# Optimization experiments

Measured on AMD Instinct MI355X. Metric: run time of the kernel, lower is better.

The kernel has to match this reference:

```python
import jax, jax.numpy as jnp
import numpy as np

REGION_DIM = 144
LLM_DIM = 3584
NUM_HEADS = 4
HEAD_DIM = REGION_DIM // NUM_HEADS          # 36
V_HEAD_DIM = LLM_DIM // NUM_HEADS           # 896
LN_EPS = 1e-5
N, M = 4096, 4096


def setup_inputs() -> dict:
    key = jax.random.key(0)
    ks = jax.random.split(key, 16)
    s = 0.02
    return {
        "target_emb": jax.random.normal(ks[0], (N, REGION_DIM), jnp.float32),
        "source_emb": jax.random.normal(ks[1], (M, LLM_DIM), jnp.float32),
        "value_emb":  jax.random.normal(ks[2], (M, LLM_DIM), jnp.float32),
        # params stored [in, out] (transposed vs torch nn.Linear)
        "wq_w": jax.random.normal(ks[3], (REGION_DIM, REGION_DIM), jnp.float32) * s,
        "wq_b": jnp.zeros((REGION_DIM,), jnp.float32),
        "wk_w": jax.random.normal(ks[4], (LLM_DIM, REGION_DIM), jnp.float32) * s,
        "wk_b": jnp.zeros((REGION_DIM,), jnp.float32),
        # per-head V projections stacked: [H, llm_dim, llm_dim//H]
        "wv_w": jax.random.normal(ks[5], (NUM_HEADS, LLM_DIM, V_HEAD_DIM), jnp.float32) * s,
        "wv_b": jnp.zeros((NUM_HEADS, V_HEAD_DIM), jnp.float32),
        "resid_w": jax.random.normal(ks[6], (REGION_DIM, LLM_DIM), jnp.float32) * s,
        "resid_b": jnp.zeros((LLM_DIM,), jnp.float32),
        "out_w": jax.random.normal(ks[7], (LLM_DIM, LLM_DIM), jnp.float32) * s,
        "out_b": jnp.zeros((LLM_DIM,), jnp.float32),
        "ln_g": jnp.ones((LLM_DIM,), jnp.float32),
        "ln_b": jnp.zeros((LLM_DIM,), jnp.float32),
    }


def reference(target_emb, source_emb, value_emb,
              wq_w, wq_b, wk_w, wk_b, wv_w, wv_b,
              resid_w, resid_b, out_w, out_b, ln_g, ln_b):
    n = target_emb.shape[0]
    # Q: [N, region_dim] -> [H, N, head_dim]; K: [M, llm_dim] -> [H, M, head_dim]
    Q = (target_emb @ wq_w + wq_b).reshape(n, NUM_HEADS, HEAD_DIM).transpose(1, 0, 2)
    K = (source_emb @ wk_w + wk_b).reshape(-1, NUM_HEADS, HEAD_DIM).transpose(1, 0, 2)
    scores = jnp.einsum('hnd,hmd->hnm', Q, K) / jnp.sqrt(jnp.float32(HEAD_DIM))
    attn = jax.nn.softmax(scores, axis=-1)      # dropout = identity (eval mode)
    # per-head value projections: [H, M, llm_dim//H]
    V = jnp.einsum('me,hed->hmd', value_emb, wv_w) + wv_b[:, None, :]
    ctx = jnp.einsum('hnm,hmd->nhd', attn, V).reshape(n, LLM_DIM)
    x = ctx + (target_emb @ resid_w + resid_b)   # residual_proj (region_dim != llm_dim)
    mu = jnp.mean(x, axis=-1, keepdims=True)
    var = jnp.mean(jnp.square(x - mu), axis=-1, keepdims=True)
    x = (x - mu) * jax.lax.rsqrt(var + LN_EPS) * ln_g + ln_b
    return x @ out_w + out_b
```

## Files before the change

### kernel.cpp

```cpp
#include <hip/hip_runtime.h>

typedef _Float16 f16;
typedef _Float16 f16x8 __attribute__((ext_vector_type(8)));
typedef float f32x4 __attribute__((ext_vector_type(4)));

#define REGION_DIM 144
#define LLM_DIM 3584
#define NUM_HEADS 4
#define HEAD_DIM 36
#define HEAD_PAD 64
#define QK_COLS 256
#define KPAD_REGION 160
#define V_HEAD 896
#define LN_EPS 1e-5f

__device__ __forceinline__ void gl_lds16(const f16* g, f16* l)
{
    __builtin_amdgcn_global_load_lds(
        (const __attribute__((address_space(1))) unsigned int*)g,
        (__attribute__((address_space(3))) unsigned int*)l, 16, 0, 0);
}

#define S_BARRIER() do { asm volatile("" ::: "memory"); __builtin_amdgcn_s_barrier(); asm volatile("" ::: "memory"); } while (0)
#define SCHED_FENCE() __builtin_amdgcn_sched_barrier(0)

__global__ void k_convert_pad(const float* __restrict__ in, f16* __restrict__ out,
                              int Cin, int Cout)
{
    int r = blockIdx.y;
    int c = blockIdx.x * 256 + threadIdx.x;
    if (c >= Cout) return;
    float v = (c < Cin) ? in[(long)r * Cin + c] : 0.f;
    out[(long)r * Cout + c] = (f16)v;
}

__global__ void k_transpose(const float* __restrict__ in, f16* __restrict__ out,
                            int R, int C, int Rpad, int Cpad,
                            long in_bstride, long out_bstride)
{
    __shared__ float tile[32][33];
    const float* ip = in + (long)blockIdx.z * in_bstride;
    f16* op = out + (long)blockIdx.z * out_bstride;
    int r0 = blockIdx.y * 32, c0 = blockIdx.x * 32;
    int tx = threadIdx.x, ty = threadIdx.y;
#pragma unroll
    for (int i = 0; i < 32; i += 8) {
        int r = r0 + ty + i, c = c0 + tx;
        tile[ty + i][tx] = (r < R && c < C) ? ip[(long)r * C + c] : 0.f;
    }
    __syncthreads();
#pragma unroll
    for (int i = 0; i < 32; i += 8) {
        int c = c0 + ty + i, r = r0 + tx;
        if (c < Cpad && r < Rpad) op[(long)c * Rpad + r] = (f16)tile[tx][ty + i];
    }
}

__global__ void k_headpad_w(const float* __restrict__ w, const float* __restrict__ b,
                            f16* __restrict__ outW, float* __restrict__ outB,
                            int E, int Epad)
{
    int hp = blockIdx.y;
    int h = hp >> 6, kk = hp & 63;
    int d = h * HEAD_DIM + kk;
    bool valid = (kk < HEAD_DIM);
    int e = blockIdx.x * 256 + threadIdx.x;
    if (e < Epad) {
        float v = (valid && e < E) ? w[(long)e * REGION_DIM + d] : 0.f;
        outW[(long)hp * Epad + e] = (f16)v;
    }
    if (blockIdx.x == 0 && threadIdx.x == 0) outB[hp] = valid ? b[d] : 0.f;
}

enum { EPI_F16_EXPSCALE = 0,
       EPI_F16_BIASROW  = 1,
       EPI_F16_DIVROW   = 2,
       EPI_F32_BIASCOL  = 3,
       EPI_F16_BIASCOL  = 4,
       EPI_F16_EXPSUM   = 5 };

template <int EPI>
__global__ __launch_bounds__(256, 2)
void gemm_f16(const f16* __restrict__ A, int lda, long sAz,
              const f16* __restrict__ Bt, int ldb, long sBz,
              void* __restrict__ Cv, int ldc, long sCz,
              const float* __restrict__ bias, long sbz, float scale, int K,
              float* __restrict__ rowpart)
{
    __shared__ __align__(16) f16 sA[128 * 32];
    __shared__ __align__(16) f16 sB[128 * 32];
    __shared__ float ps[256];
    const int tid = threadIdx.x;
    const int z = blockIdx.z;
    A += (long)z * sAz;
    Bt += (long)z * sBz;
    if (bias) bias += (long)z * sbz;

    const int gx = gridDim.x, gy = gridDim.y;
    int pid = blockIdx.y * gx + blockIdx.x;
    const int GROUP = 8;
    int span = GROUP * gx;
    int gid = pid / span;
    int y0 = gid * GROUP;
    int gsz = (gy - y0 < GROUP) ? (gy - y0) : GROUP;
    int rem = pid - gid * span;
    const int by = y0 + rem % gsz;
    const int bx = rem / gsz;
    const int m0 = by * 128, n0 = bx * 128;

    const int w = tid >> 6, l = tid & 63;
    const int wu = __builtin_amdgcn_readfirstlane(w);
    const int wr = w >> 1, wc = w & 1;

    f32x4 acc[4][4] = {};

    const int srow = tid >> 2;
    const int scol = (tid & 3) * 8;
    const f16* Ag = A + (long)(m0 + srow) * lda + scol;
    const f16* Bg = Bt + (long)(n0 + srow) * ldb + scol;
    f16* sA0 = sA + wu * 512;
    f16* sA1 = sA + 2048 + wu * 512;
    f16* sB0 = sB + wu * 512;
    f16* sB1 = sB + 2048 + wu * 512;
    const int qk = (l >> 4) * 8;
    const int fr = l & 15;

    for (int k0 = 0; k0 < K; k0 += 32) {
        __syncthreads();
        gl_lds16(Ag + k0, sA0);
        gl_lds16(Ag + (long)64 * lda + k0, sA1);
        gl_lds16(Bg + k0, sB0);
        gl_lds16(Bg + (long)64 * ldb + k0, sB1);
        __syncthreads();

        f16x8 af[4], bf[4];
#pragma unroll
        for (int mt = 0; mt < 4; mt++)
            af[mt] = *(const f16x8*)&sA[(wr * 64 + mt * 16 + fr) * 32 + qk];
#pragma unroll
        for (int nt = 0; nt < 4; nt++)
            bf[nt] = *(const f16x8*)&sB[(wc * 64 + nt * 16 + fr) * 32 + qk];
#pragma unroll
        for (int mt = 0; mt < 4; mt++)
#pragma unroll
            for (int nt = 0; nt < 4; nt++)
                acc[mt][nt] = __builtin_amdgcn_mfma_f32_16x16x32_f16(af[mt], bf[nt], acc[mt][nt], 0, 0, 0);
    }

    const int q4 = (l >> 4) * 4;
    float bc[4];
#pragma unroll
    for (int nt = 0; nt < 4; nt++) {
        if constexpr (EPI == EPI_F16_BIASCOL || EPI == EPI_F32_BIASCOL)
            bc[nt] = bias[n0 + wc * 64 + nt * 16 + fr];
        else
            bc[nt] = 0.f;
    }
    float rsum[4][4];
    if constexpr (EPI == EPI_F16_EXPSUM) {
#pragma unroll
        for (int a = 0; a < 4; a++)
#pragma unroll
            for (int b = 0; b < 4; b++) rsum[a][b] = 0.f;
    }
#pragma unroll
    for (int mt = 0; mt < 4; mt++)
#pragma unroll
        for (int r = 0; r < 4; r++) {
            int row = m0 + wr * 64 + mt * 16 + q4 + r;
            float rowv = 0.f;
            if constexpr (EPI == EPI_F16_BIASROW) rowv = bias[row];
            if constexpr (EPI == EPI_F16_DIVROW) rowv = 1.f / bias[row];
#pragma unroll
            for (int nt = 0; nt < 4; nt++) {
                int col = n0 + wc * 64 + nt * 16 + fr;
                float v = acc[mt][nt][r];
                if constexpr (EPI == EPI_F16_EXPSCALE || EPI == EPI_F16_EXPSUM) {
                    float e = __expf(v * scale);
                    ((f16*)Cv + (long)z * sCz)[(long)row * ldc + col] = (f16)e;
                    if constexpr (EPI == EPI_F16_EXPSUM) rsum[mt][r] += e;
                } else if constexpr (EPI == EPI_F16_BIASROW) {
                    ((f16*)Cv + (long)z * sCz)[(long)row * ldc + col] = (f16)(v + rowv);
                } else if constexpr (EPI == EPI_F16_DIVROW) {
                    ((f16*)Cv + (long)z * sCz)[(long)row * ldc + col] = (f16)(v * rowv);
                } else if constexpr (EPI == EPI_F16_BIASCOL) {
                    ((f16*)Cv + (long)z * sCz)[(long)row * ldc + col] = (f16)(v + bc[nt]);
                } else {
                    ((float*)Cv + (long)z * sCz)[(long)row * ldc + col] = v + bc[nt];
                }
            }
        }

    if constexpr (EPI == EPI_F16_EXPSUM) {
#pragma unroll
        for (int mt = 0; mt < 4; mt++)
#pragma unroll
            for (int r = 0; r < 4; r++) {
                float s = rsum[mt][r];
                s += __shfl_xor(s, 1);
                s += __shfl_xor(s, 2);
                s += __shfl_xor(s, 4);
                s += __shfl_xor(s, 8);
                if (fr == 0) ps[wc * 128 + wr * 64 + mt * 16 + q4 + r] = s;
            }
        __syncthreads();
        if (tid < 128) {
            long rows = (long)gy * 128;
            rowpart[((long)z * gx + bx) * rows + m0 + tid] = ps[tid] + ps[128 + tid];
        }
    }
}

template <int EPI>
__global__ __launch_bounds__(512, 2)
void gemm256_f16(const f16* __restrict__ A, int lda,
                 const f16* __restrict__ Bt, int ldb,
                 void* __restrict__ Cv, int ldc,
                 const float* __restrict__ bias, int K)
{
    __shared__ __align__(16) f16 sm[65536];
    f16* smf = sm;

    const int tid = threadIdx.x;
    const int l = tid & 63;

    const int gx = gridDim.x, gy = gridDim.y;
    int pid = blockIdx.y * gx + blockIdx.x;
    int nwg = gx * gy;
    int q = nwg >> 3, r8 = nwg & 7;
    int xcd = pid & 7, idx = pid >> 3;
    int swz = (xcd < r8) ? (xcd * (q + 1) + idx)
                         : (r8 * (q + 1) + (xcd - r8) * q + idx);
    const int by = swz % gy, bx = swz / gy;
    const int m0 = by * 256, n0 = bx * 256;

    const int wu = __builtin_amdgcn_readfirstlane(tid >> 6);
    const int wr = wu >> 2;
    const int wc = wu & 3;
    const int wst = wu * 512;

    const int strow = wu * 8 + (l >> 3);
    const int stcol = ((l & 7) ^ (l >> 3)) * 8;
    const f16* Asrc = A + (size_t)(m0 + strow) * lda + stcol;
    const f16* Bsrc = Bt + (size_t)(n0 + strow) * ldb + stcol;

    const int fr = l & 15;
    const int hi8 = (l >> 4) * 8;
    const int swl = (fr & 7) * 8;
    const int ca0 = hi8 ^ swl;
    const int ca1 = (32 + hi8) ^ swl;

    const int NT = K >> 6;

    f32x4 acc[8][4] = {};
    f16x8 af0[4][2], af1[4][2], bf0[2][2], bf1[2][2];

    gl_lds16(Asrc, smf + wst);
    gl_lds16(Asrc + (size_t)64 * lda, smf + 4096 + wst);
    gl_lds16(Asrc + (size_t)128 * lda, smf + 8192 + wst);
    gl_lds16(Asrc + (size_t)192 * lda, smf + 8192 + 4096 + wst);
    gl_lds16(Bsrc, smf + 16384 + wst);
    gl_lds16(Bsrc + (size_t)64 * ldb, smf + 16384 + 4096 + wst);
    gl_lds16(Bsrc + (size_t)128 * ldb, smf + 16384 + 8192 + wst);
    gl_lds16(Bsrc + (size_t)192 * ldb, smf + 16384 + 8192 + 4096 + wst);
    if (NT > 1) {
        gl_lds16(Bsrc + 64, smf + 32768 + 16384 + wst);
        gl_lds16(Bsrc + 64 + (size_t)64 * ldb, smf + 32768 + 16384 + 4096 + wst);
        gl_lds16(Asrc + 64, smf + 32768 + wst);
        gl_lds16(Asrc + 64 + (size_t)64 * lda, smf + 32768 + 4096 + wst);
        asm volatile("s_waitcnt vmcnt(4)" ::: "memory");
    } else {
        asm volatile("s_waitcnt vmcnt(0)" ::: "memory");
    }
    S_BARRIER();
    {
        const f16* sAp0 = smf + wr * 8192 + fr * 64;
#pragma unroll
        for (int i = 0; i < 4; i++) {
            af0[i][0] = *(const f16x8*)(sAp0 + i * 1024 + ca0);
            af0[i][1] = *(const f16x8*)(sAp0 + i * 1024 + ca1);
        }
    }

#define MFMA_Q(MB, NB, AF, BF)                                                        \
    _Pragma("unroll") for (int i = 0; i < 4; i++)                                     \
    _Pragma("unroll") for (int j = 0; j < 2; j++) {                                   \
        acc[MB + i][NB + j] = __builtin_amdgcn_mfma_f32_16x16x32_f16(                 \
            AF[i][0], BF[j][0], acc[MB + i][NB + j], 0, 0, 0);                        \
        acc[MB + i][NB + j] = __builtin_amdgcn_mfma_f32_16x16x32_f16(                 \
            AF[i][1], BF[j][1], acc[MB + i][NB + j], 0, 0, 0);                        \
    }

    for (int t = 0; t < NT; ++t) {
        const int p = t & 1;
        const f16* sAp = smf + (p << 15) + wr * 8192 + fr * 64;
        const f16* sBp = smf + (p << 15) + 16384 + wc * 4096 + fr * 64;
        const bool s1 = (t + 1 < NT), s2 = (t + 2 < NT);

#pragma unroll
        for (int j = 0; j < 2; j++) {
            bf0[j][0] = *(const f16x8*)(sBp + j * 1024 + ca0);
            bf0[j][1] = *(const f16x8*)(sBp + j * 1024 + ca1);
        }
#pragma unroll
        for (int j = 0; j < 2; j++) {
            bf1[j][0] = *(const f16x8*)(sBp + 2048 + j * 1024 + ca0);
            bf1[j][1] = *(const f16x8*)(sBp + 2048 + j * 1024 + ca1);
        }
        if (s1) {
            const f16* sa = Asrc + (size_t)128 * lda + (size_t)(t + 1) * 64;
            f16* da = smf + ((p ^ 1) << 15) + 8192 + wst;
            gl_lds16(sa, da);
            gl_lds16(sa + (size_t)64 * lda, da + 4096);
            const f16* sb = Bsrc + (size_t)128 * ldb + (size_t)(t + 1) * 64;
            f16* db = smf + ((p ^ 1) << 15) + 16384 + 8192 + wst;
            gl_lds16(sb, db);
            gl_lds16(sb + (size_t)64 * ldb, db + 4096);
        }
        asm volatile("s_waitcnt lgkmcnt(4)" ::: "memory");
        SCHED_FENCE();
        __builtin_amdgcn_s_setprio(1);
        MFMA_Q(0, 0, af0, bf0);
        __builtin_amdgcn_s_setprio(0);

#pragma unroll
        for (int i = 0; i < 4; i++) {
            af1[i][0] = *(const f16x8*)(sAp + 4096 + i * 1024 + ca0);
            af1[i][1] = *(const f16x8*)(sAp + 4096 + i * 1024 + ca1);
        }
        asm volatile("s_waitcnt lgkmcnt(8)" ::: "memory");
        SCHED_FENCE();
        __builtin_amdgcn_s_setprio(1);
        MFMA_Q(0, 2, af0, bf1);
        __builtin_amdgcn_s_setprio(0);

        S_BARRIER();
        if (s2) {
            const f16* sb = Bsrc + (size_t)(t + 2) * 64;
            f16* db = smf + (p << 15) + 16384 + wst;
            gl_lds16(sb, db);
            gl_lds16(sb + (size_t)64 * ldb, db + 4096);
        }
        asm volatile("s_waitcnt lgkmcnt(0)" ::: "memory");
        SCHED_FENCE();
        __builtin_amdgcn_s_setprio(1);
        MFMA_Q(4, 2, af1, bf1);
        __builtin_amdgcn_s_setprio(0);

        S_BARRIER();
        if (s2) {
            const f16* sa = Asrc + (size_t)(t + 2) * 64;
            f16* da = smf + (p << 15) + wst;
            gl_lds16(sa, da);
            gl_lds16(sa + (size_t)64 * lda, da + 4096);
            asm volatile("s_waitcnt vmcnt(4)" ::: "memory");
        } else if (s1) {
            asm volatile("s_waitcnt vmcnt(0)" ::: "memory");
        }
        if (s1) {
            S_BARRIER();
            const f16* sApN = smf + ((p ^ 1) << 15) + wr * 8192 + fr * 64;
#pragma unroll
            for (int i = 0; i < 4; i++) {
                af0[i][0] = *(const f16x8*)(sApN + i * 1024 + ca0);
                af0[i][1] = *(const f16x8*)(sApN + i * 1024 + ca1);
            }
        }
        __builtin_amdgcn_s_setprio(1);
        MFMA_Q(4, 0, af1, bf0);
        __builtin_amdgcn_s_setprio(0);
    }
#undef MFMA_Q

    const int q4 = (l >> 4) * 4;
    float bc[4];
#pragma unroll
    for (int nt = 0; nt < 4; nt++) {
        if constexpr (EPI == EPI_F16_BIASCOL || EPI == EPI_F32_BIASCOL)
            bc[nt] = bias[n0 + wc * 64 + nt * 16 + fr];
        else
            bc[nt] = 0.f;
    }
#pragma unroll
    for (int mt = 0; mt < 8; mt++)
#pragma unroll
        for (int r = 0; r < 4; r++) {
            int row = m0 + wr * 128 + mt * 16 + q4 + r;
            float rowv = 0.f;
            if constexpr (EPI == EPI_F16_BIASROW) rowv = bias[row];
            if constexpr (EPI == EPI_F16_DIVROW) rowv = 1.f / bias[row];
#pragma unroll
            for (int nt = 0; nt < 4; nt++) {
                int col = n0 + wc * 64 + nt * 16 + fr;
                float v = acc[mt][nt][r];
                if constexpr (EPI == EPI_F16_BIASROW) {
                    ((f16*)Cv)[(size_t)row * ldc + col] = (f16)(v + rowv);
                } else if constexpr (EPI == EPI_F16_DIVROW) {
                    ((f16*)Cv)[(size_t)row * ldc + col] = (f16)(v * rowv);
                } else if constexpr (EPI == EPI_F16_BIASCOL) {
                    ((f16*)Cv)[(size_t)row * ldc + col] = (f16)(v + bc[nt]);
                } else {
                    ((float*)Cv)[(size_t)row * ldc + col] = v + bc[nt];
                }
            }
        }
}

__global__ __launch_bounds__(512, 2)
void gemm_pv(const f16* __restrict__ A, int lda, long sAz,
             const f16* __restrict__ Bt, int ldb, long sBz,
             f16* __restrict__ C, int ldc, long sCz,
             const float* __restrict__ lsum, long slz, int K)
{
    __shared__ __align__(16) f16 sm[49152];
    const int tid = threadIdx.x;
    const int l = tid & 63;
    const int z = blockIdx.z;
    A += (size_t)z * sAz;
    Bt += (size_t)z * sBz;
    C += (size_t)z * sCz;
    lsum += (size_t)z * slz;

    const int gx = gridDim.x, gy = gridDim.y;
    int pid = blockIdx.y * gx + blockIdx.x;
    int nwg = gx * gy;
    int q = nwg >> 3, r8 = nwg & 7;
    int xcd = pid & 7, idx = pid >> 3;
    int swz = (xcd < r8) ? (xcd * (q + 1) + idx)
                         : (r8 * (q + 1) + (xcd - r8) * q + idx);
    const int by = swz % gy, bx = swz / gy;
    const int m0 = by * 256, n0 = bx * 128;

    const int wu = __builtin_amdgcn_readfirstlane(tid >> 6);
    const int wr = wu >> 1;
    const int wc = wu & 1;
    const int wst = wu * 512;

    const int strow = wu * 8 + (l >> 3);
    const int stcol = ((l & 7) ^ (l >> 3)) * 8;
    const f16* Asrc = A + (size_t)(m0 + strow) * lda + stcol;
    const f16* Bsrc = Bt + (size_t)(n0 + strow) * ldb + stcol;

    const int fr = l & 15;
    const int hi8 = (l >> 4) * 8;
    const int swl = (fr & 7) * 8;
    const int ca0 = hi8 ^ swl;
    const int ca1 = (32 + hi8) ^ swl;

    const int NT = K >> 6;

    f32x4 acc[4][4] = {};
    f16x8 af[4][2], bf0[2][2], bf1[2][2];

#define PV_STAGE(TT, B)                                                        \
    do {                                                                       \
        f16* base_ = sm + (B) * 24576;                                         \
        const f16* a_ = Asrc + (size_t)(TT) * 64;                              \
        gl_lds16(a_, base_ + wst);                                             \
        gl_lds16(a_ + (size_t)64 * lda, base_ + 4096 + wst);                   \
        gl_lds16(a_ + (size_t)128 * lda, base_ + 8192 + wst);                  \
        gl_lds16(a_ + (size_t)192 * lda, base_ + 12288 + wst);                 \
        const f16* b_ = Bsrc + (size_t)(TT) * 64;                              \
        gl_lds16(b_, base_ + 16384 + wst);                                     \
        gl_lds16(b_ + (size_t)64 * ldb, base_ + 20480 + wst);                  \
    } while (0)

    PV_STAGE(0, 0);
    PV_STAGE(1, 1);
    asm volatile("s_waitcnt vmcnt(6)" ::: "memory");
    S_BARRIER();

    for (int t = 0; t < NT; ++t) {
        const int p = t & 1;
        const f16* sAp = sm + p * 24576 + wr * 4096 + fr * 64;
        const f16* sBp = sm + p * 24576 + 16384 + wc * 4096 + fr * 64;
        const bool s1 = (t + 1 < NT), s2 = (t + 2 < NT);

#pragma unroll
        for (int i = 0; i < 4; i++) {
            af[i][0] = *(const f16x8*)(sAp + i * 1024 + ca0);
            af[i][1] = *(const f16x8*)(sAp + i * 1024 + ca1);
        }
#pragma unroll
        for (int j = 0; j < 2; j++) {
            bf0[j][0] = *(const f16x8*)(sBp + j * 1024 + ca0);
            bf0[j][1] = *(const f16x8*)(sBp + j * 1024 + ca1);
        }
#pragma unroll
        for (int j = 0; j < 2; j++) {
            bf1[j][0] = *(const f16x8*)(sBp + 2048 + j * 1024 + ca0);
            bf1[j][1] = *(const f16x8*)(sBp + 2048 + j * 1024 + ca1);
        }
        asm volatile("s_waitcnt lgkmcnt(4)" ::: "memory");
        SCHED_FENCE();
        __builtin_amdgcn_s_setprio(1);
#pragma unroll
        for (int i = 0; i < 4; i++)
#pragma unroll
            for (int j = 0; j < 2; j++) {
                acc[i][j] = __builtin_amdgcn_mfma_f32_16x16x32_f16(af[i][0], bf0[j][0], acc[i][j], 0, 0, 0);
                acc[i][j] = __builtin_amdgcn_mfma_f32_16x16x32_f16(af[i][1], bf0[j][1], acc[i][j], 0, 0, 0);
            }
        __builtin_amdgcn_s_setprio(0);
        asm volatile("s_waitcnt lgkmcnt(0)" ::: "memory");
        SCHED_FENCE();
        S_BARRIER();
        if (s2) {
            PV_STAGE(t + 2, p);
            asm volatile("s_waitcnt vmcnt(6)" ::: "memory");
        } else if (s1) {
            asm volatile("s_waitcnt vmcnt(0)" ::: "memory");
        }
        S_BARRIER();
        __builtin_amdgcn_s_setprio(1);
#pragma unroll
        for (int i = 0; i < 4; i++)
#pragma unroll
            for (int j = 0; j < 2; j++) {
                acc[i][2 + j] = __builtin_amdgcn_mfma_f32_16x16x32_f16(af[i][0], bf1[j][0], acc[i][2 + j], 0, 0, 0);
                acc[i][2 + j] = __builtin_amdgcn_mfma_f32_16x16x32_f16(af[i][1], bf1[j][1], acc[i][2 + j], 0, 0, 0);
            }
        __builtin_amdgcn_s_setprio(0);
    }
#undef PV_STAGE

    const int q4 = (l >> 4) * 4;
#pragma unroll
    for (int mt = 0; mt < 4; mt++)
#pragma unroll
        for (int r = 0; r < 4; r++) {
            int row = m0 + wr * 64 + mt * 16 + q4 + r;
            float rowv = 1.f / lsum[row];
#pragma unroll
            for (int nt = 0; nt < 4; nt++) {
                int col = n0 + wc * 64 + nt * 16 + fr;
                C[(size_t)row * ldc + col] = (f16)(acc[mt][nt][r] * rowv);
            }
        }
}

__global__ void k_partred(const float* __restrict__ part, float* __restrict__ lsum,
                          int nb, int n)
{
    int i = blockIdx.x * 256 + threadIdx.x;
    int z = i / n, r = i - z * n;
    float s = 0.f;
    for (int j = 0; j < nb; j++) s += part[((long)z * nb + j) * n + r];
    lsum[i] = s;
}

__global__ void k_layernorm(const f16* __restrict__ ctxp, const f16* __restrict__ resp,
                            const float* __restrict__ g, const float* __restrict__ be,
                            f16* __restrict__ out)
{
    long base = (long)blockIdx.x * LLM_DIM;
    const f16x8* c8 = (const f16x8*)(ctxp + base);
    const f16x8* r8 = (const f16x8*)(resp + base);
    int t = threadIdx.x, w = t >> 6, l = t & 63;
    bool has2 = t < 192;
    f16x8 a0 = c8[t], b0 = r8[t];
    f16x8 a1 = {}, b1 = {};
    if (has2) { a1 = c8[256 + t]; b1 = r8[256 + t]; }
    float v[16];
    float s = 0.f;
#pragma unroll
    for (int j = 0; j < 8; j++) { v[j] = (float)a0[j] + (float)b0[j]; s += v[j]; }
#pragma unroll
    for (int j = 0; j < 8; j++) v[8 + j] = (float)a1[j] + (float)b1[j];
    if (has2)
#pragma unroll
        for (int j = 0; j < 8; j++) s += v[8 + j];
#pragma unroll
    for (int o = 32; o; o >>= 1) s += __shfl_xor(s, o);
    __shared__ float r1[4];
    if (l == 0) r1[w] = s;
    __syncthreads();
    float mu = (r1[0] + r1[1] + r1[2] + r1[3]) * (1.f / LLM_DIM);
    float s2 = 0.f;
#pragma unroll
    for (int j = 0; j < 8; j++) { float d = v[j] - mu; s2 += d * d; }
    if (has2)
#pragma unroll
        for (int j = 8; j < 16; j++) { float d = v[j] - mu; s2 += d * d; }
#pragma unroll
    for (int o = 32; o; o >>= 1) s2 += __shfl_xor(s2, o);
    __shared__ float r2[4];
    if (l == 0) r2[w] = s2;
    __syncthreads();
    float var = (r2[0] + r2[1] + r2[2] + r2[3]) * (1.f / LLM_DIM);
    float inv = rsqrtf(var + LN_EPS);
    f16* op = out + base;
    f16x8 o0, o1;
#pragma unroll
    for (int j = 0; j < 8; j++) {
        int c = t * 8 + j;
        o0[j] = (f16)((v[j] - mu) * inv * g[c] + be[c]);
    }
    ((f16x8*)op)[t] = o0;
    if (has2) {
#pragma unroll
        for (int j = 0; j < 8; j++) {
            int c = (256 + t) * 8 + j;
            o1[j] = (f16)((v[8 + j] - mu) * inv * g[c] + be[c]);
        }
        ((f16x8*)op)[256 + t] = o1;
    }
}

extern "C" void kernel_launch(void* const* d_in, const int* in_sizes, int n_in,
                              void* d_out, int out_size, void* d_ws, size_t ws_size,
                              hipStream_t stream)
{
    const float* target  = (const float*)d_in[0];
    const float* source  = (const float*)d_in[1];
    const float* value   = (const float*)d_in[2];
    const float* wq_w    = (const float*)d_in[3];
    const float* wq_b    = (const float*)d_in[4];
    const float* wk_w    = (const float*)d_in[5];
    const float* wk_b    = (const float*)d_in[6];
    const float* wv_w    = (const float*)d_in[7];
    const float* wv_b    = (const float*)d_in[8];
    const float* resid_w = (const float*)d_in[9];
    const float* resid_b = (const float*)d_in[10];
    const float* out_w   = (const float*)d_in[11];
    const float* out_b   = (const float*)d_in[12];
    const float* ln_g    = (const float*)d_in[13];
    const float* ln_b    = (const float*)d_in[14];

    const int N = in_sizes[0] / REGION_DIM;
    const int M = in_sizes[1] / LLM_DIM;

    char* ws = (char*)d_ws;
    size_t off = 0;
    auto alloc = [&](size_t bytes) { void* p = ws + off; off += (bytes + 255) & ~(size_t)255; return p; };
    f16*   tgt16   = (f16*)alloc((size_t)N * KPAD_REGION * 2);
    f16*   residT  = (f16*)alloc((size_t)LLM_DIM * KPAD_REGION * 2);
    f16*   outT    = (f16*)alloc((size_t)LLM_DIM * LLM_DIM * 2);
    f16*   wqT     = (f16*)alloc((size_t)QK_COLS * KPAD_REGION * 2);
    float* biasK   = (float*)alloc(QK_COLS * 4);
    float* biasQ   = (float*)alloc(QK_COLS * 4);
    f16*   Qtmp    = (f16*)alloc((size_t)N * QK_COLS * 2);
    f16*   Ktmp    = (f16*)alloc((size_t)M * QK_COLS * 2);
    f16*   Vt      = (f16*)alloc((size_t)LLM_DIM * M * 2);
    f16*   residbf = (f16*)alloc((size_t)N * LLM_DIM * 2);
    f16*   ctx     = (f16*)alloc((size_t)N * LLM_DIM * 2);
    f16*   xln     = (f16*)alloc((size_t)N * LLM_DIM * 2);
    float* lsum    = (float*)alloc((size_t)2 * N * 4);
    float* rowpart = (float*)alloc((size_t)2 * (M / 128) * N * 4);
    const int HB = 2;
    char* U = (char*)alloc((size_t)HB * N * M * 2);
    f16* val16 = (f16*)U;
    f16* wvT   = (f16*)(U + (size_t)M * LLM_DIM * 2);
    f16* src16 = (f16*)U;
    f16* wkT   = (f16*)(U + (size_t)M * LLM_DIM * 2);
    f16* attnB = (f16*)U;
    (void)n_in; (void)out_size; (void)ws_size;

    dim3 tb(32, 8);

    k_convert_pad<<<dim3(1, N), 256, 0, stream>>>(target, tgt16, REGION_DIM, KPAD_REGION);
    k_transpose<<<dim3(LLM_DIM / 32, KPAD_REGION / 32, 1), tb, 0, stream>>>(
        resid_w, residT, REGION_DIM, LLM_DIM, KPAD_REGION, LLM_DIM, 0, 0);
    k_transpose<<<dim3(LLM_DIM / 32, LLM_DIM / 32, 1), tb, 0, stream>>>(
        out_w, outT, LLM_DIM, LLM_DIM, LLM_DIM, LLM_DIM, 0, 0);
    k_headpad_w<<<dim3(1, QK_COLS), 256, 0, stream>>>(wq_w, wq_b, wqT, biasQ, REGION_DIM, KPAD_REGION);

    gemm_f16<EPI_F16_BIASCOL><<<dim3(QK_COLS / 128, N / 128), 256, 0, stream>>>(
        tgt16, KPAD_REGION, 0, wqT, KPAD_REGION, 0, Qtmp, QK_COLS, 0, biasQ, 0, 1.f, KPAD_REGION, nullptr);
    gemm_f16<EPI_F16_BIASCOL><<<dim3(LLM_DIM / 128, N / 128), 256, 0, stream>>>(
        tgt16, KPAD_REGION, 0, residT, KPAD_REGION, 0, residbf, LLM_DIM, 0, resid_b, 0, 1.f, KPAD_REGION, nullptr);

    k_convert_pad<<<dim3(LLM_DIM / 256, M), 256, 0, stream>>>(value, val16, LLM_DIM, LLM_DIM);
    k_transpose<<<dim3(V_HEAD / 32, LLM_DIM / 32, NUM_HEADS), tb, 0, stream>>>(
        wv_w, wvT, LLM_DIM, V_HEAD, LLM_DIM, V_HEAD, (long)LLM_DIM * V_HEAD, (long)V_HEAD * LLM_DIM);
    gemm256_f16<EPI_F16_BIASROW><<<dim3(M / 256, LLM_DIM / 256), 512, 0, stream>>>(
        wvT, LLM_DIM, val16, LLM_DIM, Vt, M, wv_b, LLM_DIM);

    k_convert_pad<<<dim3(LLM_DIM / 256, M), 256, 0, stream>>>(source, src16, LLM_DIM, LLM_DIM);
    k_headpad_w<<<dim3(LLM_DIM / 256, QK_COLS), 256, 0, stream>>>(wk_w, wk_b, wkT, biasK, LLM_DIM, LLM_DIM);
    gemm_f16<EPI_F16_BIASCOL><<<dim3(QK_COLS / 128, M / 128), 256, 0, stream>>>(
        src16, LLM_DIM, 0, wkT, LLM_DIM, 0, Ktmp, QK_COLS, 0, biasK, 0, 1.f, LLM_DIM, nullptr);

    const float sc = 0.16666667f;
    for (int h0 = 0; h0 < NUM_HEADS; h0 += HB) {
        gemm_f16<EPI_F16_EXPSUM><<<dim3(M / 128, N / 128, HB), 256, 0, stream>>>(
            Qtmp + h0 * HEAD_PAD, QK_COLS, HEAD_PAD,
            Ktmp + h0 * HEAD_PAD, QK_COLS, HEAD_PAD,
            attnB, M, (long)N * M, nullptr, 0, sc, HEAD_PAD, rowpart);
        k_partred<<<(2 * N) / 256, 256, 0, stream>>>(rowpart, lsum, M / 128, N);
        gemm_pv<<<dim3(V_HEAD / 128, N / 256, HB), 512, 0, stream>>>(
            attnB, M, (long)N * M,
            Vt + (size_t)h0 * V_HEAD * M, M, (long)V_HEAD * M,
            ctx + (size_t)h0 * V_HEAD, LLM_DIM, V_HEAD, lsum, N, M);
    }

    k_layernorm<<<N, 256, 0, stream>>>(ctx, residbf, ln_g, ln_b, xln);
    gemm256_f16<EPI_F32_BIASCOL><<<dim3(LLM_DIM / 256, N / 256), 512, 0, stream>>>(
        xln, LLM_DIM, outT, LLM_DIM, (float*)d_out, LLM_DIM, out_b, LLM_DIM);
}
```

Before: 804.0 us.

## Triple-buffer PV GEMM, fuse row-sum reduction, and simplify gemm256 prefetch staging

The PV GEMM moves from double to triple buffering in LDS, issuing the t+2 stage at the top of each iteration so one barrier per iteration replaces two. The separate partial-row-sum reduction kernel is removed, and each PV block sums its rows' partials into shared memory itself. gemm256 now prefetches whole A/B stages at once instead of splitting half-tiles across phases. The larger LDS footprint (about 147KB for the PV kernel) may limit occupancy, and the per-block row-sum is recomputed by every column block.

Result: slower. 841.4 us (+4.7%).

```diff
diff --git a/kernel.cpp b/kernel.cpp
--- a/kernel.cpp
+++ b/kernel.cpp
@@ -255,20 +255,31 @@
     f32x4 acc[8][4] = {};
     f16x8 af0[4][2], af1[4][2], bf0[2][2], bf1[2][2];
 
-    gl_lds16(Asrc, smf + wst);
-    gl_lds16(Asrc + (size_t)64 * lda, smf + 4096 + wst);
-    gl_lds16(Asrc + (size_t)128 * lda, smf + 8192 + wst);
-    gl_lds16(Asrc + (size_t)192 * lda, smf + 8192 + 4096 + wst);
-    gl_lds16(Bsrc, smf + 16384 + wst);
-    gl_lds16(Bsrc + (size_t)64 * ldb, smf + 16384 + 4096 + wst);
-    gl_lds16(Bsrc + (size_t)128 * ldb, smf + 16384 + 8192 + wst);
-    gl_lds16(Bsrc + (size_t)192 * ldb, smf + 16384 + 8192 + 4096 + wst);
+#define G_STAGE_A(TT, P)                                                       \
+    do {                                                                       \
+        const f16* a_ = Asrc + (size_t)(TT) * 64;                              \
+        f16* d_ = smf + ((P) << 15) + wst;                                     \
+        gl_lds16(a_, d_);                                                      \
+        gl_lds16(a_ + (size_t)64 * lda, d_ + 4096);                            \
+        gl_lds16(a_ + (size_t)128 * lda, d_ + 8192);                           \
+        gl_lds16(a_ + (size_t)192 * lda, d_ + 12288);                          \
+    } while (0)
+#define G_STAGE_B(TT, P)                                                       \
+    do {                                                                       \
+        const f16* b_ = Bsrc + (size_t)(TT) * 64;                              \
+        f16* d_ = smf + ((P) << 15) + 16384 + wst;                             \
+        gl_lds16(b_, d_);                                                      \
+        gl_lds16(b_ + (size_t)64 * ldb, d_ + 4096);                            \
+        gl_lds16(b_ + (size_t)128 * ldb, d_ + 8192);                           \
+        gl_lds16(b_ + (size_t)192 * ldb, d_ + 12288);                          \
+    } while (0)
+
+    G_STAGE_A(0, 0);
+    G_STAGE_B(0, 0);
     if (NT > 1) {
-        gl_lds16(Bsrc + 64, smf + 32768 + 16384 + wst);
-        gl_lds16(Bsrc + 64 + (size_t)64 * ldb, smf + 32768 + 16384 + 4096 + wst);
-        gl_lds16(Asrc + 64, smf + 32768 + wst);
-        gl_lds16(Asrc + 64 + (size_t)64 * lda, smf + 32768 + 4096 + wst);
-        asm volatile("s_waitcnt vmcnt(4)" ::: "memory");
+        G_STAGE_A(1, 1);
+        G_STAGE_B(1, 1);
+        asm volatile("s_waitcnt vmcnt(8)" ::: "memory");
     } else {
         asm volatile("s_waitcnt vmcnt(0)" ::: "memory");
     }
@@ -307,16 +318,6 @@
             bf1[j][0] = *(const f16x8*)(sBp + 2048 + j * 1024 + ca0);
             bf1[j][1] = *(const f16x8*)(sBp + 2048 + j * 1024 + ca1);
         }
-        if (s1) {
-            const f16* sa = Asrc + (size_t)128 * lda + (size_t)(t + 1) * 64;
-            f16* da = smf + ((p ^ 1) << 15) + 8192 + wst;
-            gl_lds16(sa, da);
-            gl_lds16(sa + (size_t)64 * lda, da + 4096);
-            const f16* sb = Bsrc + (size_t)128 * ldb + (size_t)(t + 1) * 64;
-            f16* db = smf + ((p ^ 1) << 15) + 16384 + 8192 + wst;
-            gl_lds16(sb, db);
-            gl_lds16(sb + (size_t)64 * ldb, db + 4096);
-        }
         asm volatile("s_waitcnt lgkmcnt(4)" ::: "memory");
         SCHED_FENCE();
         __builtin_amdgcn_s_setprio(1);
@@ -335,12 +336,7 @@
         __builtin_amdgcn_s_setprio(0);
 
         S_BARRIER();
-        if (s2) {
-            const f16* sb = Bsrc + (size_t)(t + 2) * 64;
-            f16* db = smf + (p << 15) + 16384 + wst;
-            gl_lds16(sb, db);
-            gl_lds16(sb + (size_t)64 * ldb, db + 4096);
-        }
+        if (s2) G_STAGE_B(t + 2, p);
         asm volatile("s_waitcnt lgkmcnt(0)" ::: "memory");
         SCHED_FENCE();
         __builtin_amdgcn_s_setprio(1);
@@ -348,12 +344,9 @@
         __builtin_amdgcn_s_setprio(0);
 
         S_BARRIER();
+        if (s2) G_STAGE_A(t + 2, p);
         if (s2) {
-            const f16* sa = Asrc + (size_t)(t + 2) * 64;
-            f16* da = smf + (p << 15) + wst;
-            gl_lds16(sa, da);
-            gl_lds16(sa + (size_t)64 * lda, da + 4096);
-            asm volatile("s_waitcnt vmcnt(4)" ::: "memory");
+            asm volatile("s_waitcnt vmcnt(8)" ::: "memory");
         } else if (s1) {
             asm volatile("s_waitcnt vmcnt(0)" ::: "memory");
         }
@@ -371,6 +364,8 @@
         __builtin_amdgcn_s_setprio(0);
     }
 #undef MFMA_Q
+#undef G_STAGE_A
+#undef G_STAGE_B
 
     const int q4 = (l >> 4) * 4;
     float bc[4];
@@ -410,16 +405,17 @@
 void gemm_pv(const f16* __restrict__ A, int lda, long sAz,
              const f16* __restrict__ Bt, int ldb, long sBz,
              f16* __restrict__ C, int ldc, long sCz,
-             const float* __restrict__ lsum, long slz, int K)
-{
-    __shared__ __align__(16) f16 sm[49152];
+             const float* __restrict__ rowpart, long rpz, int nb, int nrows,
+             int K)
+{
+    __shared__ __align__(16) f16 sm[73728];
+    __shared__ float lsums[256];
     const int tid = threadIdx.x;
     const int l = tid & 63;
     const int z = blockIdx.z;
     A += (size_t)z * sAz;
     Bt += (size_t)z * sBz;
     C += (size_t)z * sCz;
-    lsum += (size_t)z * slz;
 
     const int gx = gridDim.x, gy = gridDim.y;
     int pid = blockIdx.y * gx + blockIdx.x;
@@ -465,16 +461,30 @@
         gl_lds16(b_ + (size_t)64 * ldb, base_ + 20480 + wst);                  \
     } while (0)
 
+    if (tid < 256) {
+        float s = 0.f;
+        const float* rp = rowpart + (size_t)z * rpz + (m0 + tid);
+        for (int j = 0; j < nb; j++) s += rp[(size_t)j * nrows];
+        lsums[tid] = s;
+    }
+
     PV_STAGE(0, 0);
-    PV_STAGE(1, 1);
-    asm volatile("s_waitcnt vmcnt(6)" ::: "memory");
+    if (NT > 1) {
+        PV_STAGE(1, 1);
+        asm volatile("s_waitcnt vmcnt(6)" ::: "memory");
+    } else {
+        asm volatile("s_waitcnt vmcnt(0)" ::: "memory");
+    }
     S_BARRIER();
 
+    int b = 0;
     for (int t = 0; t < NT; ++t) {
-        const int p = t & 1;
-        const f16* sAp = sm + p * 24576 + wr * 4096 + fr * 64;
-        const f16* sBp = sm + p * 24576 + 16384 + wc * 4096 + fr * 64;
-        const bool s1 = (t + 1 < NT), s2 = (t + 2 < NT);
+        if (t + 2 < NT) {
+            int b2 = b + 2; if (b2 >= 3) b2 -= 3;
+            PV_STAGE(t + 2, b2);
+        }
+        const f16* sAp = sm + b * 24576 + wr * 4096 + fr * 64;
+        const f16* sBp = sm + b * 24576 + 16384 + wc * 4096 + fr * 64;
 
 #pragma unroll
         for (int i = 0; i < 4; i++) {
@@ -504,14 +514,6 @@
         __builtin_amdgcn_s_setprio(0);
         asm volatile("s_waitcnt lgkmcnt(0)" ::: "memory");
         SCHED_FENCE();
-        S_BARRIER();
-        if (s2) {
-            PV_STAGE(t + 2, p);
-            asm volatile("s_waitcnt vmcnt(6)" ::: "memory");
-        } else if (s1) {
-            asm volatile("s_waitcnt vmcnt(0)" ::: "memory");
-        }
-        S_BARRIER();
         __builtin_amdgcn_s_setprio(1);
 #pragma unroll
         for (int i = 0; i < 4; i++)
@@ -521,6 +523,15 @@
                 acc[i][2 + j] = __builtin_amdgcn_mfma_f32_16x16x32_f16(af[i][1], bf1[j][1], acc[i][2 + j], 0, 0, 0);
             }
         __builtin_amdgcn_s_setprio(0);
+        if (t + 1 < NT) {
+            if (t + 2 < NT) {
+                asm volatile("s_waitcnt vmcnt(6)" ::: "memory");
+            } else {
+                asm volatile("s_waitcnt vmcnt(0)" ::: "memory");
+            }
+            S_BARRIER();
+        }
+        if (++b == 3) b = 0;
     }
 #undef PV_STAGE
 
@@ -529,24 +540,15 @@
     for (int mt = 0; mt < 4; mt++)
 #pragma unroll
         for (int r = 0; r < 4; r++) {
-            int row = m0 + wr * 64 + mt * 16 + q4 + r;
-            float rowv = 1.f / lsum[row];
+            int ro = wr * 64 + mt * 16 + q4 + r;
+            int row = m0 + ro;
+            float rowv = 1.f / lsums[ro];
 #pragma unroll
             for (int nt = 0; nt < 4; nt++) {
                 int col = n0 + wc * 64 + nt * 16 + fr;
                 C[(size_t)row * ldc + col] = (f16)(acc[mt][nt][r] * rowv);
             }
         }
-}
-
-__global__ void k_partred(const float* __restrict__ part, float* __restrict__ lsum,
-                          int nb, int n)
-{
-    int i = blockIdx.x * 256 + threadIdx.x;
-    int z = i / n, r = i - z * n;
-    float s = 0.f;
-    for (int j = 0; j < nb; j++) s += part[((long)z * nb + j) * n + r];
-    lsum[i] = s;
 }
 
 __global__ void k_layernorm(const f16* __restrict__ ctxp, const f16* __restrict__ resp,
@@ -645,7 +647,6 @@
     f16*   residbf = (f16*)alloc((size_t)N * LLM_DIM * 2);
     f16*   ctx     = (f16*)alloc((size_t)N * LLM_DIM * 2);
     f16*   xln     = (f16*)alloc((size_t)N * LLM_DIM * 2);
-    float* lsum    = (float*)alloc((size_t)2 * N * 4);
     float* rowpart = (float*)alloc((size_t)2 * (M / 128) * N * 4);
     const int HB = 2;
     char* U = (char*)alloc((size_t)HB * N * M * 2);
@@ -687,11 +688,11 @@
             Qtmp + h0 * HEAD_PAD, QK_COLS, HEAD_PAD,
             Ktmp + h0 * HEAD_PAD, QK_COLS, HEAD_PAD,
             attnB, M, (long)N * M, nullptr, 0, sc, HEAD_PAD, rowpart);
-        k_partred<<<(2 * N) / 256, 256, 0, stream>>>(rowpart, lsum, M / 128, N);
         gemm_pv<<<dim3(V_HEAD / 128, N / 256, HB), 512, 0, stream>>>(
             attnB, M, (long)N * M,
             Vt + (size_t)h0 * V_HEAD * M, M, (long)V_HEAD * M,
-            ctx + (size_t)h0 * V_HEAD, LLM_DIM, V_HEAD, lsum, N, M);
+            ctx + (size_t)h0 * V_HEAD, LLM_DIM, V_HEAD,
+            rowpart, (long)(M / 128) * N, M / 128, N, M);
     }
 
     k_layernorm<<<N, 256, 0, stream>>>(ctx, residbf, ln_g, ln_b, xln);
```
